# Kernel tuning notes

Measured on AMD Instinct MI355X. Metric: run time of the kernel, lower is better.

Reference implementation:

```python
import jax, jax.numpy as jnp
import numpy as np
from jax import lax


def conv2d(x, w, pad):
    return lax.conv_general_dilated(x, w, (1, 1), [(pad, pad), (pad, pad)],
                                    dimension_numbers=('NCHW', 'OIHW', 'NCHW'))


def deform_conv2d(x, offset, w, b, k, pad):
    # torchvision-style DeformConv2d, stride 1, dilation 1, 1 group.
    # offset: [B, 2*k*k, H, W], pairs ordered (dy, dx) per kernel tap (row-major).
    B, C, H, W = x.shape
    KK = k * k
    off = offset.reshape(B, KK, 2, H, W)
    ky, kx = jnp.meshgrid(jnp.arange(k), jnp.arange(k), indexing='ij')
    ky = ky.reshape(1, KK, 1, 1).astype(x.dtype)
    kx = kx.reshape(1, KK, 1, 1).astype(x.dtype)
    gy = jnp.arange(H, dtype=x.dtype).reshape(1, 1, H, 1)
    gx = jnp.arange(W, dtype=x.dtype).reshape(1, 1, 1, W)
    ys = gy + ky - pad + off[:, :, 0]  # [B, KK, H, W]
    xs = gx + kx - pad + off[:, :, 1]
    y0 = jnp.floor(ys)
    x0 = jnp.floor(xs)
    y1 = y0 + 1.0
    x1 = x0 + 1.0
    img = x.reshape(B, C, H * W)

    def corner(yc, xc, wt):
        # zero padding outside the image
        valid = (yc >= 0) & (yc <= H - 1) & (xc >= 0) & (xc <= W - 1)
        idx = (jnp.clip(yc, 0, H - 1) * W + jnp.clip(xc, 0, W - 1)).astype(jnp.int32).reshape(B, -1)
        g = jax.vmap(lambda im, ix: jnp.take(im, ix, axis=1))(img, idx)  # [B, C, KK*H*W]
        return g.reshape(B, C, KK, H, W) * (wt * valid)[:, None]

    v = (corner(y0, x0, (y1 - ys) * (x1 - xs))
         + corner(y0, x1, (y1 - ys) * (xs - x0))
         + corner(y1, x0, (ys - y0) * (x1 - xs))
         + corner(y1, x1, (ys - y0) * (xs - x0)))  # [B, C, KK, H, W]
    out = jnp.einsum('bckhw,ock->bohw', v, w.reshape(w.shape[0], C, KK))
    return out + b[None, :, None, None]


def setup_inputs() -> dict:
    key = jax.random.key(0)
    ks = jax.random.split(key, 16)
    f32 = jnp.float32
    dim = 64

    def rn(k, shape, s):
        return jax.random.normal(k, shape, f32) * s

    return {
        'x': rn(ks[0], (4, dim, 96, 96), 1.0),
        'w_off3': rn(ks[1], (18, dim, 3, 3), 0.01), 'b_off3': jnp.zeros((18,), f32),
        'w_off5': rn(ks[2], (50, dim, 3, 3), 0.01), 'b_off5': jnp.zeros((50,), f32),
        'w_off7': rn(ks[3], (98, dim, 3, 3), 0.01), 'b_off7': jnp.zeros((98,), f32),
        'w_d3': rn(ks[4], (dim, dim, 3, 3), 0.04), 'b_d3': rn(ks[5], (dim,), 0.01),
        'w_d5': rn(ks[6], (dim, dim, 5, 5), 0.025), 'b_d5': rn(ks[7], (dim,), 0.01),
        'w_d7': rn(ks[8], (dim, dim, 7, 7), 0.018), 'b_d7': rn(ks[9], (dim,), 0.01),
        'w_sp': rn(ks[10], (1, 2, 7, 7), 0.1),
        'w_ca1': rn(ks[11], (12, 3 * dim, 1, 1), 0.07),
        'w_ca2': rn(ks[12], (3 * dim, 12, 1, 1), 0.28),
    }


def reference(x, w_off3, b_off3, w_off5, b_off5, w_off7, b_off7,
              w_d3, b_d3, w_d5, b_d5, w_d7, b_d7, w_sp, w_ca1, w_ca2):
    off3 = conv2d(x, w_off3, 1) + b_off3[None, :, None, None]
    off5 = conv2d(x, w_off5, 1) + b_off5[None, :, None, None]
    off7 = conv2d(x, w_off7, 1) + b_off7[None, :, None, None]
    a1 = deform_conv2d(x, off3, w_d3, b_d3, 3, 1)
    a2 = deform_conv2d(x, off5, w_d5, b_d5, 5, 2)
    a3 = deform_conv2d(x, off7, w_d7, b_d7, 7, 3)
    res = jnp.concatenate([a1, a2, a3], axis=1)  # [B, 3C, H, W]

    # SpatialAttention: channel mean/max -> 7x7 conv -> sigmoid
    sp_in = jnp.concatenate([jnp.mean(res, axis=1, keepdims=True),
                             jnp.max(res, axis=1, keepdims=True)], axis=1)
    sp = jax.nn.sigmoid(conv2d(sp_in, w_sp, 3))  # [B, 1, H, W]

    # ChannelAttention: shared MLP on avg- and max-pooled descriptors
    def fc(t):
        return conv2d(jnp.maximum(conv2d(t, w_ca1, 0), 0.0), w_ca2, 0)

    avg = jnp.mean(res, axis=(2, 3), keepdims=True)
    mx = jnp.max(res, axis=(2, 3), keepdims=True)
    ch = jax.nn.sigmoid(fc(avg) + fc(mx))  # [B, 3C, 1, 1]

    C = x.shape[1]
    c1, c2, c3 = ch[:, :C], ch[:, C:2 * C], ch[:, 2 * C:]
    return a1 * (sp + c1) + a2 * (sp + c2) + a3 * (sp + c3)
```

## Files before the change

kernel.cpp:

```cpp
#include <hip/hip_runtime.h>
#include <math.h>

#define H 96
#define W 96
#define HW (H*W)
#define CIN 64
#define NB 4
#define NOFF 166
#define OFFROW 168

typedef __attribute__((ext_vector_type(8)))  short short8;
typedef __attribute__((ext_vector_type(8)))  _Float16 half8;
typedef __attribute__((ext_vector_type(16))) float f32x16;
typedef unsigned short ushort_t;

static const size_t OFF_ALL = 0;
static const size_t RES     = OFF_ALL + (size_t)NB*HW*OFFROW;
static const size_t XB16    = RES + (size_t)NB*192*HW;
static const size_t WTD3    = XB16 + (size_t)NB*64*HW/2;
static const size_t WTD5    = WTD3 + 9*4096/2;
static const size_t WTD7    = WTD5 + 25*4096/2;
static const size_t WOFF    = WTD7 + 49*4096/2;
static const size_t BOFF    = WOFF + 9*192*64/2;
static const size_t SPIN    = BOFF + 192;
static const size_t SPATT   = SPIN + (size_t)NB*2*HW;
static const size_t POOLAVG = SPATT + (size_t)NB*HW;
static const size_t POOLMAX = POOLAVG + NB*192;
static const size_t CHATT   = POOLMAX + NB*192;

__device__ __forceinline__ ushort_t f2h(float f) {
    _Float16 h = (_Float16)f;
    return __builtin_bit_cast(unsigned short, h);
}
__device__ __forceinline__ half8 as_h8(short8 s) {
    return __builtin_bit_cast(half8, s);
}
__device__ __forceinline__ half8 splat8(float f) {
    _Float16 h = (_Float16)f;
    half8 v;
    #pragma unroll
    for (int j = 0; j < 8; j++) v[j] = h;
    return v;
}

__global__ __launch_bounds__(256) void convert_x_nhwc_kernel(const float* __restrict__ x,
                                                             ushort_t* __restrict__ xb) {
    __shared__ ushort_t tile[64][66];
    int t = threadIdx.x;
    int b = blockIdx.x / 144;
    int p0 = (blockIdx.x % 144) * 64;
    int q = t >> 6, ln = t & 63;
    #pragma unroll
    for (int i = 0; i < 16; i++) {
        int c = q * 16 + i;
        tile[ln][c] = f2h(x[((size_t)(b * 64 + c)) * HW + p0 + ln]);
    }
    __syncthreads();
    #pragma unroll
    for (int i = 0; i < 16; i++) {
        int pos = q * 16 + i;
        xb[((size_t)b * HW + p0 + pos) * 64 + ln] = tile[pos][ln];
    }
}

__global__ void convert_wt_all_kernel(const float* __restrict__ w3, const float* __restrict__ w5,
                                      const float* __restrict__ w7,
                                      ushort_t* __restrict__ wt3, ushort_t* __restrict__ wt5,
                                      ushort_t* __restrict__ wt7) {
    int idx = blockIdx.x * 256 + threadIdx.x;
    const float* src; ushort_t* dst; int KK; int o;
    if (idx < 9 * 4096)       { src = w3; dst = wt3; KK = 9;  o = idx; }
    else if (idx < 34 * 4096) { src = w5; dst = wt5; KK = 25; o = idx - 9 * 4096; }
    else if (idx < 83 * 4096) { src = w7; dst = wt7; KK = 49; o = idx - 34 * 4096; }
    else return;
    int j    = o & 7;
    int l31  = (o >> 3) & 31;
    int lh   = (o >> 8) & 1;
    int cs   = (o >> 9) & 3;
    int half = (o >> 11) & 1;
    int kk   = o >> 12;
    int co = half * 32 + l31;
    int c  = cs * 16 + lh * 8 + j;
    dst[o] = f2h(src[((size_t)co * 64 + c) * KK + kk]);
}

__global__ void build_woff_kernel(const float* __restrict__ w3, const float* __restrict__ w5,
                                  const float* __restrict__ w7, const float* __restrict__ b3,
                                  const float* __restrict__ b5, const float* __restrict__ b7,
                                  ushort_t* __restrict__ woff, float* __restrict__ boff) {
    int idx = blockIdx.x * 256 + threadIdx.x;
    if (idx >= 9 * 192 * 64) return;
    int c  = idx & 63;
    int co = (idx >> 6) % 192;
    int kk = idx / (192 * 64);
    float v = 0.f;
    if (co < 18)       v = w3[(co * 64 + c) * 9 + kk];
    else if (co < 68)  v = w5[((co - 18) * 64 + c) * 9 + kk];
    else if (co < 166) v = w7[((co - 68) * 64 + c) * 9 + kk];
    woff[(kk * 192 + co) * 64 + c] = f2h(v);
    if (kk == 0 && c == 0) {
        float bv = 0.f;
        if (co < 18)       bv = b3[co];
        else if (co < 68)  bv = b5[co - 18];
        else if (co < 166) bv = b7[co - 68];
        boff[co] = bv;
    }
}

__global__ __launch_bounds__(256, 3) void offset_mfma_kernel(
    const ushort_t* __restrict__ xb,
    const ushort_t* __restrict__ woff,
    const float* __restrict__ bias_all,
    float* __restrict__ off_all)
{
    __shared__ float red[6144];
    const int t = threadIdx.x;
    const int lane = t & 63, l31 = lane & 31, lh = lane >> 5;
    const int wave = t >> 6;
    const int mhalf = wave >> 1, khalf = wave & 1;
    const int xcd = blockIdx.x & 7, u = blockIdx.x >> 3;
    const int b = xcd >> 1;
    const int v = u * 2 + (xcd & 1);
    const int npos = v * 32 + l31;
    const int h = npos / 96, w = npos % 96;
    const int c0 = 8 * lh;
    const ushort_t* xbase = xb + (size_t)b * HW * 64;

    f32x16 acc0, acc1, acc2;
    #pragma unroll
    for (int r = 0; r < 16; r++) { acc0[r] = 0.f; acc1[r] = 0.f; acc2[r] = 0.f; }

    const int kk0 = khalf ? 5 : 0, kk1 = khalf ? 9 : 5;
    const int mt0 = mhalf * 3;
    for (int kk = kk0; kk < kk1; kk++) {
        int ky = kk / 3, kx = kk % 3;
        int y = h + ky - 1, x = w + kx - 1;
        bool ok = ((unsigned)y < (unsigned)H) && ((unsigned)x < (unsigned)W);
        int o = ok ? (y * W + x) : 0;
        short zm = ok ? (short)0xFFFF : (short)0;
        const ushort_t* px = xbase + (size_t)o * 64 + c0;
        const ushort_t* wk = woff + (size_t)kk * 12288;
        #pragma unroll
        for (int cs = 0; cs < 4; cs++) {
            int cc = cs * 16;
            short8 q = *(const short8*)(px + cc);
            short8 bm;
            #pragma unroll
            for (int j = 0; j < 8; j++) bm[j] = (short)(q[j] & zm);
            half8 bfrag = as_h8(bm);
            half8 a0 = as_h8(*(const short8*)(wk + (size_t)((mt0 + 0) * 32 + l31) * 64 + cc + c0));
            half8 a1 = as_h8(*(const short8*)(wk + (size_t)((mt0 + 1) * 32 + l31) * 64 + cc + c0));
            half8 a2 = as_h8(*(const short8*)(wk + (size_t)((mt0 + 2) * 32 + l31) * 64 + cc + c0));
            acc0 = __builtin_amdgcn_mfma_f32_32x32x16_f16(a0, bfrag, acc0, 0, 0, 0);
            acc1 = __builtin_amdgcn_mfma_f32_32x32x16_f16(a1, bfrag, acc1, 0, 0, 0);
            acc2 = __builtin_amdgcn_mfma_f32_32x32x16_f16(a2, bfrag, acc2, 0, 0, 0);
        }
    }

    if (khalf) {
        float* rp = red + mhalf * 3072;
        #pragma unroll
        for (int r = 0; r < 16; r++) {
            rp[(0 * 16 + r) * 64 + lane] = acc0[r];
            rp[(1 * 16 + r) * 64 + lane] = acc1[r];
            rp[(2 * 16 + r) * 64 + lane] = acc2[r];
        }
    }
    __syncthreads();
    if (!khalf) {
        const float* rp = red + mhalf * 3072;
        #pragma unroll
        for (int r = 0; r < 16; r++) {
            acc0[r] += rp[(0 * 16 + r) * 64 + lane];
            acc1[r] += rp[(1 * 16 + r) * 64 + lane];
            acc2[r] += rp[(2 * 16 + r) * 64 + lane];
        }
        float* row = off_all + ((size_t)b * HW + npos) * OFFROW;
        #pragma unroll
        for (int m = 0; m < 3; m++) {
            const f32x16& a = (m == 0) ? acc0 : (m == 1) ? acc1 : acc2;
            int mt = mt0 + m;
            #pragma unroll
            for (int q = 0; q < 4; q++) {
                int base = mt * 32 + 8 * q + 4 * lh;
                if (base < 166) {
                    float4 vv = make_float4(a[4 * q + 0] + bias_all[base + 0],
                                            a[4 * q + 1] + bias_all[base + 1],
                                            a[4 * q + 2] + bias_all[base + 2],
                                            a[4 * q + 3] + bias_all[base + 3]);
                    *(float4*)(row + base) = vv;
                }
            }
        }
    }
}

__device__ __forceinline__ void store_tile(int b, int tile, int lane, int g,
                                           const float* __restrict__ bias,
                                           const f32x16& acc0, const f32x16& acc1,
                                           float* __restrict__ res)
{
    const int l31 = lane & 31, lh = lane >> 5;
    const int npos = tile * 32 + l31;
    size_t rb = (((size_t)b * 3 + g) * 64) * HW + npos;
    #pragma unroll
    for (int r = 0; r < 16; r++) {
        int co = (r & 3) + 8 * (r >> 2) + 4 * lh;
        res[rb + (size_t)co * HW]        = acc0[r] + bias[co];
        res[rb + (size_t)(co + 32) * HW] = acc1[r] + bias[co + 32];
    }
}

#define MG  5
#define PNY 12
#define PNX 43
#define PXS 144
#define PRS (PNX * PXS)

template<int K, int PAD>
__device__ __forceinline__ void deform_span(
    const float* __restrict__ offp, const ushort_t* __restrict__ wtf,
    int kk0, int kk1, int h, int w, int w0, int l31, int lh,
    const char* lds, f32x16& acc0, f32x16& acc1)
{
    const int lh16 = lh * 16;
    const float2* offp2 = (const float2*)offp;
    float2 off = offp2[kk0];
    for (int kk = kk0; kk < kk1; kk++) {
        float2 noff = offp2[(kk + 1 < kk1) ? kk + 1 : kk];

        int ky = kk / K, kx = kk % K;
        float ys = (float)(h + ky - PAD) + off.x;
        float xs = (float)(w + kx - PAD) + off.y;
        float y0f = floorf(ys), x0f = floorf(xs);
        float fy = ys - y0f, fx = xs - x0f;
        int iy0 = (int)y0f, ix0 = (int)x0f;
        int iy1 = iy0 + 1, ix1 = ix0 + 1;
        float oky0 = ((unsigned)iy0 < (unsigned)H) ? 1.f : 0.f;
        float oky1 = ((unsigned)iy1 < (unsigned)H) ? 1.f : 0.f;
        float okx0 = ((unsigned)ix0 < (unsigned)W) ? 1.f : 0.f;
        float okx1 = ((unsigned)ix1 < (unsigned)W) ? 1.f : 0.f;
        float w00 = (1.f - fy) * (1.f - fx) * oky0 * okx0;
        float w01 = (1.f - fy) * fx * oky0 * okx1;
        float w10 = fy * (1.f - fx) * oky1 * okx0;
        float w11 = fy * fx * oky1 * okx1;
        int cy0 = min(max(iy0, 0), H - 1), cy1 = min(max(iy1, 0), H - 1);
        int cx0 = min(max(ix0, 0), W - 1), cx1 = min(max(ix1, 0), W - 1);
        int r0 = min(max(cy0 - h + MG, 0), PNY - 1);
        int r1 = min(max(cy1 - h + MG, 0), PNY - 1);
        int p0 = min(max(cx0 - w0 + MG, 0), PNX - 1);
        int p1 = min(max(cx1 - w0 + MG, 0), PNX - 1);
        const char* b00 = lds + r0 * PRS + p0 * PXS + lh16;
        const char* b01 = lds + r0 * PRS + p1 * PXS + lh16;
        const char* b10 = lds + r1 * PRS + p0 * PXS + lh16;
        const char* b11 = lds + r1 * PRS + p1 * PXS + lh16;

        half8 W00 = splat8(w00), W01 = splat8(w01);
        half8 W10 = splat8(w10), W11 = splat8(w11);
        const ushort_t* wkf = wtf + (size_t)kk * 4096;
        #pragma unroll
        for (int cs = 0; cs < 4; cs++) {
            half8 q00 = *(const half8*)(b00 + cs * 32);
            half8 q01 = *(const half8*)(b01 + cs * 32);
            half8 q10 = *(const half8*)(b10 + cs * 32);
            half8 q11 = *(const half8*)(b11 + cs * 32);
            half8 bfrag = q00 * W00 + q01 * W01 + q10 * W10 + q11 * W11;
            half8 a0 = as_h8(*(const short8*)(wkf + (size_t)(((0 * 4 + cs) * 2 + lh) * 32 + l31) * 8));
            half8 a1 = as_h8(*(const short8*)(wkf + (size_t)(((1 * 4 + cs) * 2 + lh) * 32 + l31) * 8));
            acc0 = __builtin_amdgcn_mfma_f32_32x32x16_f16(a0, bfrag, acc0, 0, 0, 0);
            acc1 = __builtin_amdgcn_mfma_f32_32x32x16_f16(a1, bfrag, acc1, 0, 0, 0);
        }
        off = noff;
    }
}

__global__ __launch_bounds__(256, 2) void deform_fused_kernel(
    const ushort_t* __restrict__ xb, const float* __restrict__ off_all,
    const ushort_t* __restrict__ wt3, const ushort_t* __restrict__ wt5,
    const ushort_t* __restrict__ wt7,
    const float* __restrict__ b3, const float* __restrict__ b5,
    const float* __restrict__ b7,
    float* __restrict__ res)
{
    __shared__ __align__(16) char lds[PNY * PNX * PXS];
    const int t = threadIdx.x;
    const int wave = t >> 6, lane = t & 63;
    const int xcd = blockIdx.x & 7, u = blockIdx.x >> 3;
    const int b = xcd >> 1;
    const int tile = u * 2 + (xcd & 1);

    const int l31 = lane & 31, lh = lane >> 5;
    const int h  = tile / 3;
    const int w0 = (tile % 3) * 32;
    const int w  = w0 + l31;
    const int npos = h * 96 + w;

    const ushort_t* xsrc = xb + (size_t)b * HW * 64;
    constexpr int NCH = PNY * PNX * 8;
    constexpr int NITER = (NCH + 255) / 256;
    #pragma unroll
    for (int it = 0; it < NITER; it++) {
        int c = t + it * 256;
        if (c < NCH) {
            int rr  = c / (PNX * 8);
            int rem = c - rr * (PNX * 8);
            int pp  = rem >> 3, sub = rem & 7;
            int cy = min(max(h - MG + rr, 0), H - 1);
            int cx = min(max(w0 - MG + pp, 0), W - 1);
            *(float4*)(lds + rr * PRS + pp * PXS + sub * 16) =
                *(const float4*)(xsrc + ((size_t)(cy * W + cx)) * 64 + sub * 8);
        }
    }
    __syncthreads();

    const float* offrow = off_all + ((size_t)b * HW + npos) * OFFROW;

    f32x16 a0A, a1A, a0B, a1B;
    #pragma unroll
    for (int r = 0; r < 16; r++) { a0A[r] = 0.f; a1A[r] = 0.f; a0B[r] = 0.f; a1B[r] = 0.f; }

    if (wave == 0) {
        deform_span<3, 1>(offrow + 0,  wt3, 0, 9,  h, w, w0, l31, lh, lds, a0A, a1A);
        deform_span<5, 2>(offrow + 18, wt5, 0, 12, h, w, w0, l31, lh, lds, a0B, a1B);
    } else if (wave == 1) {
        deform_span<5, 2>(offrow + 18, wt5, 12, 25, h, w, w0, l31, lh, lds, a0A, a1A);
        deform_span<7, 3>(offrow + 68, wt7, 0, 8,   h, w, w0, l31, lh, lds, a0B, a1B);
    } else if (wave == 2) {
        deform_span<7, 3>(offrow + 68, wt7, 8, 29,  h, w, w0, l31, lh, lds, a0A, a1A);
    } else {
        deform_span<7, 3>(offrow + 68, wt7, 29, 49, h, w, w0, l31, lh, lds, a0A, a1A);
    }

    __syncthreads();
    float* slots = (float*)lds;
    if (wave == 1) {
        float* s0 = slots;
        float* s1 = slots + 2048;
        #pragma unroll
        for (int r = 0; r < 16; r++) {
            s0[r * 64 + lane]        = a0A[r];
            s0[(16 + r) * 64 + lane] = a1A[r];
            s1[r * 64 + lane]        = a0B[r];
            s1[(16 + r) * 64 + lane] = a1B[r];
        }
    } else if (wave == 3) {
        float* s2 = slots + 4096;
        #pragma unroll
        for (int r = 0; r < 16; r++) {
            s2[r * 64 + lane]        = a0A[r];
            s2[(16 + r) * 64 + lane] = a1A[r];
        }
    }
    __syncthreads();
    if (wave == 0) {
        store_tile(b, tile, lane, 0, b3, a0A, a1A, res);
        const float* s0 = slots;
        #pragma unroll
        for (int r = 0; r < 16; r++) {
            a0B[r] += s0[r * 64 + lane];
            a1B[r] += s0[(16 + r) * 64 + lane];
        }
        store_tile(b, tile, lane, 1, b5, a0B, a1B, res);
    } else if (wave == 2) {
        const float* s1 = slots + 2048;
        const float* s2 = slots + 4096;
        #pragma unroll
        for (int r = 0; r < 16; r++) {
            a0A[r] += s1[r * 64 + lane] + s2[r * 64 + lane];
            a1A[r] += s1[(16 + r) * 64 + lane] + s2[(16 + r) * 64 + lane];
        }
        store_tile(b, tile, lane, 2, b7, a0A, a1A, res);
    }
}

__global__ void sp_meanmax_kernel(const float* __restrict__ res,
                                  float* __restrict__ spin) {
    int idx = blockIdx.x * 256 + threadIdx.x;
    int hw = idx % HW;
    int b  = idx / HW;
    const float* r = res + (size_t)b * 192 * HW + hw;
    float s = 0.f, m = -3.402823466e+38f;
    for (int c = 0; c < 192; c++) {
        float v = r[(size_t)c * HW];
        s += v;
        m = fmaxf(m, v);
    }
    spin[(size_t)b * 2 * HW + hw]      = s * (1.f / 192.f);
    spin[(size_t)b * 2 * HW + HW + hw] = m;
}

__global__ void sp_conv_kernel(const float* __restrict__ spin,
                               const float* __restrict__ w_sp,
                               float* __restrict__ sp) {
    int idx = blockIdx.x * 256 + threadIdx.x;
    int w = idx % W;
    int h = (idx / W) % H;
    int b = idx / HW;
    float acc = 0.f;
    for (int ci = 0; ci < 2; ci++) {
        const float* pin = spin + ((size_t)b * 2 + ci) * HW;
        const float* wp  = w_sp + ci * 49;
        #pragma unroll
        for (int dy = 0; dy < 7; dy++) {
            int yy = h + dy - 3;
            if (yy < 0 || yy >= H) continue;
            #pragma unroll
            for (int dx = 0; dx < 7; dx++) {
                int xx = w + dx - 3;
                if (xx < 0 || xx >= W) continue;
                acc = fmaf(pin[yy * W + xx], wp[dy * 7 + dx], acc);
            }
        }
    }
    sp[idx] = 1.f / (1.f + expf(-acc));
}

__global__ void pool_kernel(const float* __restrict__ res,
                            float* __restrict__ avg, float* __restrict__ mx) {
    int bc = blockIdx.x;
    const float* r = res + (size_t)bc * HW;
    int t = threadIdx.x;
    float s = 0.f, m = -3.402823466e+38f;
    for (int i = t; i < HW; i += 256) {
        float v = r[i];
        s += v;
        m = fmaxf(m, v);
    }
    #pragma unroll
    for (int off = 32; off > 0; off >>= 1) {
        s += __shfl_down(s, off);
        m = fmaxf(m, __shfl_down(m, off));
    }
    __shared__ float ss[4], sm[4];
    int wid = t >> 6;
    if ((t & 63) == 0) { ss[wid] = s; sm[wid] = m; }
    __syncthreads();
    if (t == 0) {
        s = ss[0] + ss[1] + ss[2] + ss[3];
        m = fmaxf(fmaxf(sm[0], sm[1]), fmaxf(sm[2], sm[3]));
        avg[bc] = s * (1.f / (float)HW);
        mx[bc]  = m;
    }
}

__global__ void chatt_kernel(const float* __restrict__ avg,
                             const float* __restrict__ mx,
                             const float* __restrict__ w1,
                             const float* __restrict__ w2,
                             float* __restrict__ ch) {
    int b = blockIdx.x;
    int t = threadIdx.x;
    __shared__ float sa[192], sm_[192], h1a[12], h1m[12];
    if (t < 192) { sa[t] = avg[b * 192 + t]; sm_[t] = mx[b * 192 + t]; }
    __syncthreads();
    if (t < 12) {
        float s1 = 0.f, s2 = 0.f;
        for (int c = 0; c < 192; c++) {
            float wv = w1[t * 192 + c];
            s1 = fmaf(wv, sa[c], s1);
            s2 = fmaf(wv, sm_[c], s2);
        }
        h1a[t] = fmaxf(s1, 0.f);
        h1m[t] = fmaxf(s2, 0.f);
    }
    __syncthreads();
    if (t < 192) {
        float s = 0.f;
        #pragma unroll
        for (int j = 0; j < 12; j++)
            s = fmaf(w2[t * 12 + j], h1a[j] + h1m[j], s);
        ch[b * 192 + t] = 1.f / (1.f + expf(-s));
    }
}

__global__ void final_kernel(const float* __restrict__ res,
                             const float* __restrict__ sp,
                             const float* __restrict__ ch,
                             float* __restrict__ out) {
    int idx = blockIdx.x * 256 + threadIdx.x;
    int hw = idx % HW;
    int co = (idx / HW) % 64;
    int b  = idx / (64 * HW);
    size_t rb = (size_t)b * 192 * HW;
    float a1 = res[rb + (size_t)co * HW + hw];
    float a2 = res[rb + (size_t)(64 + co) * HW + hw];
    float a3 = res[rb + (size_t)(128 + co) * HW + hw];
    float spv = sp[(size_t)b * HW + hw];
    float c1 = ch[b * 192 + co];
    float c2 = ch[b * 192 + 64 + co];
    float c3 = ch[b * 192 + 128 + co];
    out[idx] = a1 * (spv + c1) + a2 * (spv + c2) + a3 * (spv + c3);
}

extern "C" void kernel_launch(void* const* d_in, const int* in_sizes, int n_in,
                              void* d_out, int out_size, void* d_ws, size_t ws_size,
                              hipStream_t stream) {
    const float* x      = (const float*)d_in[0];
    const float* w_off3 = (const float*)d_in[1];
    const float* b_off3 = (const float*)d_in[2];
    const float* w_off5 = (const float*)d_in[3];
    const float* b_off5 = (const float*)d_in[4];
    const float* w_off7 = (const float*)d_in[5];
    const float* b_off7 = (const float*)d_in[6];
    const float* w_d3   = (const float*)d_in[7];
    const float* b_d3   = (const float*)d_in[8];
    const float* w_d5   = (const float*)d_in[9];
    const float* b_d5   = (const float*)d_in[10];
    const float* w_d7   = (const float*)d_in[11];
    const float* b_d7   = (const float*)d_in[12];
    const float* w_sp   = (const float*)d_in[13];
    const float* w_ca1  = (const float*)d_in[14];
    const float* w_ca2  = (const float*)d_in[15];

    float* ws = (float*)d_ws;
    float* off_all = ws + OFF_ALL;
    float* res     = ws + RES;
    ushort_t* xb16 = (ushort_t*)(ws + XB16);
    ushort_t* wt3  = (ushort_t*)(ws + WTD3);
    ushort_t* wt5  = (ushort_t*)(ws + WTD5);
    ushort_t* wt7  = (ushort_t*)(ws + WTD7);
    ushort_t* woff = (ushort_t*)(ws + WOFF);
    float* boff = ws + BOFF;
    float* spin = ws + SPIN;
    float* sp   = ws + SPATT;
    float* avgp = ws + POOLAVG;
    float* mxp  = ws + POOLMAX;
    float* chp  = ws + CHATT;

    convert_x_nhwc_kernel<<<576, 256, 0, stream>>>(x, xb16);
    convert_wt_all_kernel<<<1328, 256, 0, stream>>>(w_d3, w_d5, w_d7, wt3, wt5, wt7);
    build_woff_kernel<<<432, 256, 0, stream>>>(w_off3, w_off5, w_off7,
                                               b_off3, b_off5, b_off7, woff, boff);

    offset_mfma_kernel<<<1152, 256, 0, stream>>>(xb16, woff, boff, off_all);

    deform_fused_kernel<<<1152, 256, 0, stream>>>(xb16, off_all, wt3, wt5, wt7,
                                                  b_d3, b_d5, b_d7, res);

    sp_meanmax_kernel<<<144, 256, 0, stream>>>(res, spin);
    sp_conv_kernel<<<144, 256, 0, stream>>>(spin, w_sp, sp);
    pool_kernel<<<768, 256, 0, stream>>>(res, avgp, mxp);
    chatt_kernel<<<4, 256, 0, stream>>>(avgp, mxp, w_ca1, w_ca2, chp);

    final_kernel<<<9216, 256, 0, stream>>>(res, sp, chp, (float*)d_out);
}
```

Baseline: 170.1 us.

## Process two output rows per block sharing one LDS halo tile

Each deform block now has 8 waves and covers two adjacent output rows. Both rows read from a single 12-row halo tile in LDS, with a per-row margin offset (mgr), which roughly halves the global-to-LDS staging per output row. The staging loop is restructured so each thread loads one column chunk across all rows. Launch bounds change to 512 threads with a 4-waves-per-EU hint, which tightens the register budget. The vertical margin becomes asymmetric (6 above and 5 below for the second row), so large offsets are clamped sooner.

```diff
diff --git a/kernel.cpp b/kernel.cpp
--- a/kernel.cpp
+++ b/kernel.cpp
@@ -220,7 +220,7 @@
 template<int K, int PAD>
 __device__ __forceinline__ void deform_span(
     const float* __restrict__ offp, const ushort_t* __restrict__ wtf,
-    int kk0, int kk1, int h, int w, int w0, int l31, int lh,
+    int kk0, int kk1, int h, int w, int w0, int l31, int lh, int mgr,
     const char* lds, f32x16& acc0, f32x16& acc1)
 {
     const int lh16 = lh * 16;
@@ -246,8 +246,8 @@
         float w11 = fy * fx * oky1 * okx1;
         int cy0 = min(max(iy0, 0), H - 1), cy1 = min(max(iy1, 0), H - 1);
         int cx0 = min(max(ix0, 0), W - 1), cx1 = min(max(ix1, 0), W - 1);
-        int r0 = min(max(cy0 - h + MG, 0), PNY - 1);
-        int r1 = min(max(cy1 - h + MG, 0), PNY - 1);
+        int r0 = min(max(cy0 - h + mgr, 0), PNY - 1);
+        int r1 = min(max(cy1 - h + mgr, 0), PNY - 1);
         int p0 = min(max(cx0 - w0 + MG, 0), PNX - 1);
         int p1 = min(max(cx1 - w0 + MG, 0), PNX - 1);
         const char* b00 = lds + r0 * PRS + p0 * PXS + lh16;
@@ -274,7 +274,7 @@
     }
 }
 
-__global__ __launch_bounds__(256, 2) void deform_fused_kernel(
+__global__ __launch_bounds__(512, 4) void deform_fused_kernel(
     const ushort_t* __restrict__ xb, const float* __restrict__ off_all,
     const ushort_t* __restrict__ wt3, const ushort_t* __restrict__ wt5,
     const ushort_t* __restrict__ wt7,
@@ -287,26 +287,24 @@
     const int wave = t >> 6, lane = t & 63;
     const int xcd = blockIdx.x & 7, u = blockIdx.x >> 3;
     const int b = xcd >> 1;
-    const int tile = u * 2 + (xcd & 1);
-
+    const int v = u * 2 + (xcd & 1);
+    const int rp = v / 3, ct = v % 3;
+    const int g = wave >> 2, wi = wave & 3;
+    const int h0 = rp * 2;
+    const int h  = h0 + g;
+    const int w0 = ct * 32;
     const int l31 = lane & 31, lh = lane >> 5;
-    const int h  = tile / 3;
-    const int w0 = (tile % 3) * 32;
-    const int w  = w0 + l31;
+    const int w = w0 + l31;
     const int npos = h * 96 + w;
+    const int tile = h * 3 + ct;
 
     const ushort_t* xsrc = xb + (size_t)b * HW * 64;
-    constexpr int NCH = PNY * PNX * 8;
-    constexpr int NITER = (NCH + 255) / 256;
-    #pragma unroll
-    for (int it = 0; it < NITER; it++) {
-        int c = t + it * 256;
-        if (c < NCH) {
-            int rr  = c / (PNX * 8);
-            int rem = c - rr * (PNX * 8);
-            int pp  = rem >> 3, sub = rem & 7;
-            int cy = min(max(h - MG + rr, 0), H - 1);
-            int cx = min(max(w0 - MG + pp, 0), W - 1);
+    if (t < PNX * 8) {
+        int pp = t >> 3, sub = t & 7;
+        int cx = min(max(w0 - MG + pp, 0), W - 1);
+        #pragma unroll
+        for (int rr = 0; rr < PNY; rr++) {
+            int cy = min(max(h0 - MG + rr, 0), H - 1);
             *(float4*)(lds + rr * PRS + pp * PXS + sub * 16) =
                 *(const float4*)(xsrc + ((size_t)(cy * W + cx)) * 64 + sub * 8);
         }
@@ -314,26 +312,27 @@
     __syncthreads();
 
     const float* offrow = off_all + ((size_t)b * HW + npos) * OFFROW;
+    const int mgr = MG + g;
 
     f32x16 a0A, a1A, a0B, a1B;
     #pragma unroll
     for (int r = 0; r < 16; r++) { a0A[r] = 0.f; a1A[r] = 0.f; a0B[r] = 0.f; a1B[r] = 0.f; }
 
-    if (wave == 0) {
-        deform_span<3, 1>(offrow + 0,  wt3, 0, 9,  h, w, w0, l31, lh, lds, a0A, a1A);
-        deform_span<5, 2>(offrow + 18, wt5, 0, 12, h, w, w0, l31, lh, lds, a0B, a1B);
-    } else if (wave == 1) {
-        deform_span<5, 2>(offrow + 18, wt5, 12, 25, h, w, w0, l31, lh, lds, a0A, a1A);
-        deform_span<7, 3>(offrow + 68, wt7, 0, 8,   h, w, w0, l31, lh, lds, a0B, a1B);
-    } else if (wave == 2) {
-        deform_span<7, 3>(offrow + 68, wt7, 8, 29,  h, w, w0, l31, lh, lds, a0A, a1A);
+    if (wi == 0) {
+        deform_span<3, 1>(offrow + 0,  wt3, 0, 9,  h, w, w0, l31, lh, mgr, lds, a0A, a1A);
+        deform_span<5, 2>(offrow + 18, wt5, 0, 12, h, w, w0, l31, lh, mgr, lds, a0B, a1B);
+    } else if (wi == 1) {
+        deform_span<5, 2>(offrow + 18, wt5, 12, 25, h, w, w0, l31, lh, mgr, lds, a0A, a1A);
+        deform_span<7, 3>(offrow + 68, wt7, 0, 8,   h, w, w0, l31, lh, mgr, lds, a0B, a1B);
+    } else if (wi == 2) {
+        deform_span<7, 3>(offrow + 68, wt7, 8, 29,  h, w, w0, l31, lh, mgr, lds, a0A, a1A);
     } else {
-        deform_span<7, 3>(offrow + 68, wt7, 29, 49, h, w, w0, l31, lh, lds, a0A, a1A);
-    }
-
-    __syncthreads();
-    float* slots = (float*)lds;
-    if (wave == 1) {
+        deform_span<7, 3>(offrow + 68, wt7, 29, 49, h, w, w0, l31, lh, mgr, lds, a0A, a1A);
+    }
+
+    __syncthreads();
+    float* slots = (float*)lds + (size_t)g * 6144;
+    if (wi == 1) {
         float* s0 = slots;
         float* s1 = slots + 2048;
         #pragma unroll
@@ -343,7 +342,7 @@
             s1[r * 64 + lane]        = a0B[r];
             s1[(16 + r) * 64 + lane] = a1B[r];
         }
-    } else if (wave == 3) {
+    } else if (wi == 3) {
         float* s2 = slots + 4096;
         #pragma unroll
         for (int r = 0; r < 16; r++) {
@@ -352,7 +351,7 @@
         }
     }
     __syncthreads();
-    if (wave == 0) {
+    if (wi == 0) {
         store_tile(b, tile, lane, 0, b3, a0A, a1A, res);
         const float* s0 = slots;
         #pragma unroll
@@ -361,7 +360,7 @@
             a1B[r] += s0[(16 + r) * 64 + lane];
         }
         store_tile(b, tile, lane, 1, b5, a0B, a1B, res);
-    } else if (wave == 2) {
+    } else if (wi == 2) {
         const float* s1 = slots + 2048;
         const float* s2 = slots + 4096;
         #pragma unroll
@@ -534,8 +533,8 @@
 
     offset_mfma_kernel<<<1152, 256, 0, stream>>>(xb16, woff, boff, off_all);
 
-    deform_fused_kernel<<<1152, 256, 0, stream>>>(xb16, off_all, wt3, wt5, wt7,
-                                                  b_d3, b_d5, b_d7, res);
+    deform_fused_kernel<<<576, 512, 0, stream>>>(xb16, off_all, wt3, wt5, wt7,
+                                                 b_d3, b_d5, b_d7, res);
 
     sp_meanmax_kernel<<<144, 256, 0, stream>>>(res, spin);
     sp_conv_kernel<<<144, 256, 0, stream>>>(spin, w_sp, sp);
```

Result: slower. 187.4 us (+10.2%).

## Use 2x16 pixel tiles in deform kernel to shrink LDS halo footprint

Applied to the files above, without the earlier changes.

Changes each block's 32-pixel tile from a 1x32 row strip to a 2x16 patch, and resizes the LDS halo buffer from 12x43 to 13x27 pixels. The smaller LDS footprint and launch bounds raised to 3 blocks per CU aim to increase occupancy and cut redundant halo loads from global memory. Stores to res now write 16-wide runs instead of 32, which may reduce write coalescing. The extra occupancy also tightens the register budget for the four accumulators.

```diff
diff --git a/kernel.cpp b/kernel.cpp
--- a/kernel.cpp
+++ b/kernel.cpp
@@ -195,13 +195,12 @@
     }
 }
 
-__device__ __forceinline__ void store_tile(int b, int tile, int lane, int g,
+__device__ __forceinline__ void store_tile(int b, int npos, int lane, int g,
                                            const float* __restrict__ bias,
                                            const f32x16& acc0, const f32x16& acc1,
                                            float* __restrict__ res)
 {
-    const int l31 = lane & 31, lh = lane >> 5;
-    const int npos = tile * 32 + l31;
+    const int lh = lane >> 5;
     size_t rb = (((size_t)b * 3 + g) * 64) * HW + npos;
     #pragma unroll
     for (int r = 0; r < 16; r++) {
@@ -212,15 +211,15 @@
 }
 
 #define MG  5
-#define PNY 12
-#define PNX 43
+#define PNY 13
+#define PNX 27
 #define PXS 144
 #define PRS (PNX * PXS)
 
 template<int K, int PAD>
 __device__ __forceinline__ void deform_span(
     const float* __restrict__ offp, const ushort_t* __restrict__ wtf,
-    int kk0, int kk1, int h, int w, int w0, int l31, int lh,
+    int kk0, int kk1, int h, int w, int h0, int w0, int l31, int lh,
     const char* lds, f32x16& acc0, f32x16& acc1)
 {
     const int lh16 = lh * 16;
@@ -246,8 +245,8 @@
         float w11 = fy * fx * oky1 * okx1;
         int cy0 = min(max(iy0, 0), H - 1), cy1 = min(max(iy1, 0), H - 1);
         int cx0 = min(max(ix0, 0), W - 1), cx1 = min(max(ix1, 0), W - 1);
-        int r0 = min(max(cy0 - h + MG, 0), PNY - 1);
-        int r1 = min(max(cy1 - h + MG, 0), PNY - 1);
+        int r0 = min(max(cy0 - h0 + MG, 0), PNY - 1);
+        int r1 = min(max(cy1 - h0 + MG, 0), PNY - 1);
         int p0 = min(max(cx0 - w0 + MG, 0), PNX - 1);
         int p1 = min(max(cx1 - w0 + MG, 0), PNX - 1);
         const char* b00 = lds + r0 * PRS + p0 * PXS + lh16;
@@ -274,7 +273,7 @@
     }
 }
 
-__global__ __launch_bounds__(256, 2) void deform_fused_kernel(
+__global__ __launch_bounds__(256, 3) void deform_fused_kernel(
     const ushort_t* __restrict__ xb, const float* __restrict__ off_all,
     const ushort_t* __restrict__ wt3, const ushort_t* __restrict__ wt5,
     const ushort_t* __restrict__ wt7,
@@ -288,11 +287,13 @@
     const int xcd = blockIdx.x & 7, u = blockIdx.x >> 3;
     const int b = xcd >> 1;
     const int tile = u * 2 + (xcd & 1);
-
+    const int rp = tile / 6, ct = tile % 6;
+    const int h0 = rp * 2;
+    const int w0 = ct * 16;
     const int l31 = lane & 31, lh = lane >> 5;
-    const int h  = tile / 3;
-    const int w0 = (tile % 3) * 32;
-    const int w  = w0 + l31;
+    const int lr = l31 >> 4, lc = l31 & 15;
+    const int h = h0 + lr;
+    const int w = w0 + lc;
     const int npos = h * 96 + w;
 
     const ushort_t* xsrc = xb + (size_t)b * HW * 64;
@@ -305,7 +306,7 @@
             int rr  = c / (PNX * 8);
             int rem = c - rr * (PNX * 8);
             int pp  = rem >> 3, sub = rem & 7;
-            int cy = min(max(h - MG + rr, 0), H - 1);
+            int cy = min(max(h0 - MG + rr, 0), H - 1);
             int cx = min(max(w0 - MG + pp, 0), W - 1);
             *(float4*)(lds + rr * PRS + pp * PXS + sub * 16) =
                 *(const float4*)(xsrc + ((size_t)(cy * W + cx)) * 64 + sub * 8);
@@ -320,15 +321,15 @@
     for (int r = 0; r < 16; r++) { a0A[r] = 0.f; a1A[r] = 0.f; a0B[r] = 0.f; a1B[r] = 0.f; }
 
     if (wave == 0) {
-        deform_span<3, 1>(offrow + 0,  wt3, 0, 9,  h, w, w0, l31, lh, lds, a0A, a1A);
-        deform_span<5, 2>(offrow + 18, wt5, 0, 12, h, w, w0, l31, lh, lds, a0B, a1B);
+        deform_span<3, 1>(offrow + 0,  wt3, 0, 9,  h, w, h0, w0, l31, lh, lds, a0A, a1A);
+        deform_span<5, 2>(offrow + 18, wt5, 0, 12, h, w, h0, w0, l31, lh, lds, a0B, a1B);
     } else if (wave == 1) {
-        deform_span<5, 2>(offrow + 18, wt5, 12, 25, h, w, w0, l31, lh, lds, a0A, a1A);
-        deform_span<7, 3>(offrow + 68, wt7, 0, 8,   h, w, w0, l31, lh, lds, a0B, a1B);
+        deform_span<5, 2>(offrow + 18, wt5, 12, 25, h, w, h0, w0, l31, lh, lds, a0A, a1A);
+        deform_span<7, 3>(offrow + 68, wt7, 0, 8,   h, w, h0, w0, l31, lh, lds, a0B, a1B);
     } else if (wave == 2) {
-        deform_span<7, 3>(offrow + 68, wt7, 8, 29,  h, w, w0, l31, lh, lds, a0A, a1A);
+        deform_span<7, 3>(offrow + 68, wt7, 8, 29,  h, w, h0, w0, l31, lh, lds, a0A, a1A);
     } else {
-        deform_span<7, 3>(offrow + 68, wt7, 29, 49, h, w, w0, l31, lh, lds, a0A, a1A);
+        deform_span<7, 3>(offrow + 68, wt7, 29, 49, h, w, h0, w0, l31, lh, lds, a0A, a1A);
     }
 
     __syncthreads();
@@ -353,14 +354,14 @@
     }
     __syncthreads();
     if (wave == 0) {
-        store_tile(b, tile, lane, 0, b3, a0A, a1A, res);
+        store_tile(b, npos, lane, 0, b3, a0A, a1A, res);
         const float* s0 = slots;
         #pragma unroll
         for (int r = 0; r < 16; r++) {
             a0B[r] += s0[r * 64 + lane];
             a1B[r] += s0[(16 + r) * 64 + lane];
         }
-        store_tile(b, tile, lane, 1, b5, a0B, a1B, res);
+        store_tile(b, npos, lane, 1, b5, a0B, a1B, res);
     } else if (wave == 2) {
         const float* s1 = slots + 2048;
         const float* s2 = slots + 4096;
@@ -369,7 +370,7 @@
             a0A[r] += s1[r * 64 + lane] + s2[r * 64 + lane];
             a1A[r] += s1[(16 + r) * 64 + lane] + s2[(16 + r) * 64 + lane];
         }
-        store_tile(b, tile, lane, 2, b7, a0A, a1A, res);
+        store_tile(b, npos, lane, 2, b7, a0A, a1A, res);
     }
 }
 
```

Measured after the change: 173.0 us. Within noise of the previous version (+1.7%).
